# Kernel tuning notes

Measured on AMD Instinct MI355X. Metric: run time of the kernel, lower is better.

Reference implementation:

```python
import jax, jax.numpy as jnp
import numpy as np

EPS = 1e-7

def fake_quant(x, bits):
    """Per-tensor affine fake-quantization (dnn-gating TorchRoundToBits),
    matching torch.fake_quantize_per_tensor_affine with dynamic range."""
    fp_max = jax.lax.stop_gradient(jnp.max(x))
    fp_min = jax.lax.stop_gradient(jnp.min(x))
    qmax = float(2 ** bits - 1)
    qmin = 0.0
    scale = (fp_max - fp_min) / (qmax - qmin) + EPS
    zero_point = jnp.trunc(qmin - fp_min / scale)  # int() cast in torch truncates
    q = jnp.round(x / scale + zero_point)
    qc = jnp.clip(q, qmin, qmax)
    return (qc - zero_point) * scale

def conv2d(x, w, stride=1, padding=1):
    return jax.lax.conv_general_dilated(
        x, w,
        window_strides=(stride, stride),
        padding=[(padding, padding), (padding, padding)],
        dimension_numbers=('NCHW', 'OIHW', 'NCHW'))

def setup_inputs() -> dict:
    key = jax.random.key(0)
    k1, k2 = jax.random.split(key)
    x = jax.random.normal(k1, (32, 256, 56, 56), dtype=jnp.float32)
    # kaiming-like init for a 3x3 conv with 256 in-channels
    fan_in = 256 * 3 * 3
    weight = jax.random.normal(k2, (256, 256, 3, 3), dtype=jnp.float32) / np.sqrt(fan_in)
    return {"x": x, "weight": weight}

def reference(x, weight):
    WBITS, ABITS, PGABITS = 8, 8, 4
    TH = 0.99
    w_q = fake_quant(weight, WBITS)          # quantized weights (shared by both convs)
    msb_in = fake_quant(x, PGABITS)          # low-precision (MSB) input
    msb_out = conv2d(msb_in, w_q)            # [32,256,56,56] prediction pass
    lsb_in = fake_quant(x, ABITS) - msb_in   # residual (LSB) input
    lsb_out = conv2d(lsb_in, w_q)            # high-precision correction pass
    mask = (jax.nn.sigmoid(msb_out) > TH).astype(msb_out.dtype)
    return msb_out + mask * lsb_out
```

## Files before the change

kernel.cpp:

```cpp
#include <hip/hip_runtime.h>
#include <stdint.h>
#include <stddef.h>

typedef int v4i  __attribute__((ext_vector_type(4)));
typedef int v16i __attribute__((ext_vector_type(16)));

struct QParams {
  float s4, z4, s8, z8, sw, zw;
  float s4sw, s8sw;
  int dw;
};

__device__ __forceinline__ unsigned enc_f(float f) {
  unsigned u = __float_as_uint(f);
  return (u & 0x80000000u) ? ~u : (u | 0x80000000u);
}
__device__ __forceinline__ float dec_f(unsigned e) {
  unsigned u = (e & 0x80000000u) ? (e ^ 0x80000000u) : ~e;
  return __uint_as_float(u);
}

__global__ void k_init(unsigned* mm, unsigned* zp) {
  int t = threadIdx.x;
  if (t < 128) zp[t] = 0u;
  if (t == 0) { mm[0] = 0xFFFFFFFFu; mm[1] = 0u; mm[2] = 0xFFFFFFFFu; mm[3] = 0u; }
}

__global__ void k_minmax(const float4* __restrict__ p, int n4, unsigned* mm) {
  float lmin = 3.4e38f, lmax = -3.4e38f;
  for (int i = blockIdx.x * blockDim.x + threadIdx.x; i < n4; i += gridDim.x * blockDim.x) {
    float4 v = p[i];
    lmin = fminf(lmin, fminf(fminf(v.x, v.y), fminf(v.z, v.w)));
    lmax = fmaxf(lmax, fmaxf(fmaxf(v.x, v.y), fmaxf(v.z, v.w)));
  }
  for (int off = 32; off; off >>= 1) {
    lmin = fminf(lmin, __shfl_down(lmin, off, 64));
    lmax = fmaxf(lmax, __shfl_down(lmax, off, 64));
  }
  __shared__ float smin[4], smax[4];
  int w = threadIdx.x >> 6, lane = threadIdx.x & 63;
  if (lane == 0) { smin[w] = lmin; smax[w] = lmax; }
  __syncthreads();
  if (threadIdx.x == 0) {
    float a = fminf(fminf(smin[0], smin[1]), fminf(smin[2], smin[3]));
    float b = fmaxf(fmaxf(smax[0], smax[1]), fmaxf(smax[2], smax[3]));
    atomicMin(&mm[0], enc_f(a));
    atomicMax(&mm[1], enc_f(b));
  }
}

__global__ void k_params(const unsigned* mm, QParams* q) {
  float xmin = dec_f(mm[0]), xmax = dec_f(mm[1]);
  float wmin = dec_f(mm[2]), wmax = dec_f(mm[3]);
  float s4 = (xmax - xmin) / 15.0f + 1e-7f;
  float z4 = truncf(0.0f - xmin / s4);
  float s8 = (xmax - xmin) / 255.0f + 1e-7f;
  float z8 = truncf(0.0f - xmin / s8);
  float sw = (wmax - wmin) / 255.0f + 1e-7f;
  float zw = truncf(0.0f - wmin / sw);
  q->s4 = s4; q->z4 = z4; q->s8 = s8; q->z8 = z8; q->sw = sw; q->zw = zw;
  q->s4sw = s4 * sw; q->s8sw = s8 * sw;
  q->dw = 128 - (int)zw;
}

__global__ void k_quant_w(const float* __restrict__ w, const QParams* __restrict__ q,
                          char* __restrict__ Wc) {
  int t = blockIdx.x * 256 + threadIdx.x;
  float sw = q->sw, zw = q->zw;
  const float* src = w + (size_t)t * 9;
#pragma unroll
  for (int j = 0; j < 9; ++j) {
    float qf = rintf(__fdiv_rn(src[j], sw) + zw);
    qf = fminf(fmaxf(qf, 0.0f), 255.0f);
    Wc[j * 65536 + t] = (char)((int)qf - 128);
  }
}

__global__ void k_quant_x(const float* __restrict__ x, const QParams* __restrict__ q,
                          char* __restrict__ A4, char* __restrict__ A8,
                          int* __restrict__ CS4, int* __restrict__ CS8) {
  __shared__ char sm4[56 * 257];
  __shared__ char sm8[56 * 257];
  __shared__ int cp4[56][4], cp8[56][4];
  int bx = blockIdx.x;
  int n = bx / 56, y = bx % 56;
  int tid = threadIdx.x;
  float s4 = q->s4, z4 = q->z4, s8 = q->s8, z8 = q->z8;
  const float* xrow = x + (size_t)n * 802816 + y * 56;
#pragma unroll 2
  for (int it = 0; it < 56; ++it) {
    int idx = it * 256 + tid;
    int c = idx / 56, xc = idx % 56;
    float v = xrow[(size_t)c * 3136 + xc];
    float q4 = rintf(__fdiv_rn(v, s4) + z4);
    q4 = fminf(fmaxf(q4, 0.0f), 15.0f);
    int t4 = (int)(q4 - z4);
    float q8 = rintf(__fdiv_rn(v, s8) + z8);
    q8 = fminf(fmaxf(q8, 0.0f), 255.0f);
    int t8 = (int)(q8 - z8);
    t8 = max(-128, min(127, t8));
    sm4[xc * 257 + c] = (char)t4;
    sm8[xc * 257 + c] = (char)t8;
  }
  __syncthreads();
  if (tid < 224) {
    int xc = tid >> 2, qq = tid & 3;
    const char* r4 = sm4 + xc * 257 + qq * 64;
    const char* r8 = sm8 + xc * 257 + qq * 64;
    int a = 0, b = 0;
#pragma unroll 8
    for (int c = 0; c < 64; ++c) { a += (signed char)r4[c]; b += (signed char)r8[c]; }
    cp4[xc][qq] = a; cp8[xc][qq] = b;
  }
  __syncthreads();
  int pixbase = n * 3136 + y * 56;
  if (tid < 56) {
    CS4[pixbase + tid] = cp4[tid][0] + cp4[tid][1] + cp4[tid][2] + cp4[tid][3];
    CS8[pixbase + tid] = cp8[tid][0] + cp8[tid][1] + cp8[tid][2] + cp8[tid][3];
  }
  unsigned* A4w = (unsigned*)A4;
  unsigned* A8w = (unsigned*)A8;
#pragma unroll 2
  for (int it = 0; it < 14; ++it) {
    int idx = it * 256 + tid;
    int xc = idx >> 6, wd = idx & 63;
    int sb = xc * 257 + wd * 4;
    unsigned u4 = (unsigned)(unsigned char)sm4[sb]
                | ((unsigned)(unsigned char)sm4[sb + 1] << 8)
                | ((unsigned)(unsigned char)sm4[sb + 2] << 16)
                | ((unsigned)(unsigned char)sm4[sb + 3] << 24);
    unsigned u8 = (unsigned)(unsigned char)sm8[sb]
                | ((unsigned)(unsigned char)sm8[sb + 1] << 8)
                | ((unsigned)(unsigned char)sm8[sb + 2] << 16)
                | ((unsigned)(unsigned char)sm8[sb + 3] << 24);
    size_t o = (size_t)(pixbase + xc) * 64 + wd;
    A4w[o] = u4; A8w[o] = u8;
  }
}

__global__ void k_wsum(const int* __restrict__ CS4, const int* __restrict__ CS8,
                       int* __restrict__ S4, int* __restrict__ S8) {
  int p = blockIdx.x * 256 + threadIdx.x;
  if (p >= 100352) return;
  int rem = p % 3136;
  int y = rem / 56, xc = rem % 56;
  int a = 0, b = 0;
#pragma unroll
  for (int dy = -1; dy <= 1; ++dy) {
    if ((unsigned)(y + dy) >= 56u) continue;
#pragma unroll
    for (int dx = -1; dx <= 1; ++dx) {
      if ((unsigned)(xc + dx) >= 56u) continue;
      int qq = p + dy * 56 + dx;
      a += CS4[qq]; b += CS8[qq];
    }
  }
  S4[p] = a; S8[p] = b;
}

#define GLD16(gp, lp)                                                         \
  __builtin_amdgcn_global_load_lds((const __attribute__((address_space(1))) void*)(gp), \
                                   (__attribute__((address_space(3))) void*)(lp), 16, 0, 0)

__device__ __forceinline__ float pg_merge(int a4v, int a8v, float fs4, float fs8) {
  float msb = fs4 * (float)a4v;
  float c8  = fs8 * (float)a8v;
  float lsb = c8 - msb;
  float sig = 1.0f / (1.0f + expf(-msb));
  return msb + (sig > 0.99f ? lsb : 0.0f);
}

__global__ __launch_bounds__(256, 2) void k_conv(
    const char* __restrict__ A4, const char* __restrict__ A8,
    const char* __restrict__ Wc,
    const int* __restrict__ S4, const int* __restrict__ S8,
    const QParams* __restrict__ q, const char* __restrict__ zpage,
    float* __restrict__ out) {
  __shared__ char smA4[8192], smA8[8192], smB[8192];
  const size_t ASZ = 25690112;
  int tid = threadIdx.x;
  int w = tid >> 6, lane = tid & 63;
  int m0 = blockIdx.x * 128;
  int n0 = blockIdx.y * 128;
  int wm = w >> 1, wn = w & 1;

  int chunk = lane & 3;
  int r0 = (w << 5) + (lane >> 2);
  int r1 = r0 + 16;
  int cg0 = chunk ^ ((r0 >> 1) & 3);
  int cg1 = chunk ^ ((r1 >> 1) & 3);
  int p0 = m0 + r0, p1 = m0 + r1;
  int rem0 = p0 % 3136, rem1 = p1 % 3136;
  int y0 = rem0 / 56, x0 = rem0 % 56;
  int y1 = rem1 / 56, x1 = rem1 % 56;
  const char* aBase0 = A4 + (size_t)p0 * 256 + cg0 * 16;
  const char* aBase1 = A4 + (size_t)p1 * 256 + cg1 * 16;
  const char* bBase0 = Wc + (n0 + r0) * 256 + cg0 * 16;
  const char* bBase1 = Wc + (n0 + r1) * 256 + cg1 * 16;
  const char* zp0 = zpage + chunk * 16;

  char* dA4 = smA4 + (w << 11);
  char* dA8 = smA8 + (w << 11);
  char* dB  = smB  + (w << 11);

  v16i acc4[2][2] = {}, acc8[2][2] = {};
  int r31 = lane & 31, qh = lane >> 5;

  for (int win = 0; win < 9; ++win) {
    int dy = win / 3 - 1, dx = win % 3 - 1;
    int doff = (dy * 56 + dx) * 256;
    bool v0ok = ((unsigned)(y0 + dy) < 56u) && ((unsigned)(x0 + dx) < 56u);
    bool v1ok = ((unsigned)(y1 + dy) < 56u) && ((unsigned)(x1 + dx) < 56u);
    const char* g40 = v0ok ? aBase0 + doff : zp0;
    const char* g41 = v1ok ? aBase1 + doff : zp0;
    const char* g80 = v0ok ? aBase0 + doff + ASZ : zp0;
    const char* g81 = v1ok ? aBase1 + doff + ASZ : zp0;
    const char* gB0 = bBase0 + win * 65536;
    const char* gB1 = bBase1 + win * 65536;
#pragma unroll
    for (int cs = 0; cs < 4; ++cs) {
      int c0 = cs * 64;
      GLD16(g40 + c0, dA4);
      GLD16(g41 + c0, dA4 + 1024);
      GLD16(g80 + c0, dA8);
      GLD16(g81 + c0, dA8 + 1024);
      GLD16(gB0 + c0, dB);
      GLD16(gB1 + c0, dB + 1024);
      asm volatile("s_waitcnt vmcnt(0)" ::: "memory");
      __syncthreads();
#pragma unroll
      for (int kc = 0; kc < 2; ++kc) {
        int ch = kc * 2 + qh;
        v4i a4f[2], a8f[2], bf[2];
#pragma unroll
        for (int fm = 0; fm < 2; ++fm) {
          int row = wm * 64 + fm * 32 + r31;
          int off = row * 64 + ((ch ^ ((row >> 1) & 3)) << 4);
          a4f[fm] = *(const v4i*)(smA4 + off);
          a8f[fm] = *(const v4i*)(smA8 + off);
        }
#pragma unroll
        for (int fn = 0; fn < 2; ++fn) {
          int row = wn * 64 + fn * 32 + r31;
          int off = row * 64 + ((ch ^ ((row >> 1) & 3)) << 4);
          bf[fn] = *(const v4i*)(smB + off);
        }
#pragma unroll
        for (int fm = 0; fm < 2; ++fm)
#pragma unroll
          for (int fn = 0; fn < 2; ++fn) {
            acc4[fm][fn] = __builtin_amdgcn_mfma_i32_32x32x32_i8(a4f[fm], bf[fn], acc4[fm][fn], 0, 0, 0);
            acc8[fm][fn] = __builtin_amdgcn_mfma_i32_32x32x32_i8(a8f[fm], bf[fn], acc8[fm][fn], 0, 0, 0);
          }
      }
      __syncthreads();
    }
  }

  float fs4 = q->s4sw, fs8 = q->s8sw;
  int dwv = q->dw;
#pragma unroll
  for (int fm = 0; fm < 2; ++fm)
#pragma unroll
    for (int fn = 0; fn < 2; ++fn) {
      int kout = n0 + wn * 64 + fn * 32 + r31;
      int pb = m0 + wm * 64 + fm * 32 + 4 * qh;
#pragma unroll
      for (int rg = 0; rg < 4; ++rg) {
        int pr = pb + 8 * rg;
        int4 sv4 = *(const int4*)(S4 + pr);
        int4 sv8 = *(const int4*)(S8 + pr);
        float4 res;
        res.x = pg_merge(acc4[fm][fn][rg * 4 + 0] + dwv * sv4.x,
                         acc8[fm][fn][rg * 4 + 0] + dwv * sv8.x, fs4, fs8);
        res.y = pg_merge(acc4[fm][fn][rg * 4 + 1] + dwv * sv4.y,
                         acc8[fm][fn][rg * 4 + 1] + dwv * sv8.y, fs4, fs8);
        res.z = pg_merge(acc4[fm][fn][rg * 4 + 2] + dwv * sv4.z,
                         acc8[fm][fn][rg * 4 + 2] + dwv * sv8.z, fs4, fs8);
        res.w = pg_merge(acc4[fm][fn][rg * 4 + 3] + dwv * sv4.w,
                         acc8[fm][fn][rg * 4 + 3] + dwv * sv8.w, fs4, fs8);
        int nimg = pr / 3136;
        int rem = pr - nimg * 3136;
        *(float4*)(out + (size_t)nimg * 802816 + (size_t)kout * 3136 + rem) = res;
      }
    }
}

extern "C" void kernel_launch(void* const* d_in, const int* in_sizes, int n_in,
                              void* d_out, int out_size, void* d_ws, size_t ws_size,
                              hipStream_t stream) {
  const float* x  = (const float*)d_in[0];
  const float* wt = (const float*)d_in[1];
  float* out = (float*)d_out;

  char* ws = (char*)d_ws;
  unsigned* mm = (unsigned*)ws;
  QParams* prm = (QParams*)(ws + 64);
  char* zpage = ws + 256;
  char* A4 = ws + 1024;
  const size_t ASZ = 25690112;
  char* A8 = A4 + ASZ;
  int* CS4 = (int*)(A8 + ASZ);
  int* CS8 = CS4 + 100352;
  int* S4  = CS8 + 100352;
  int* S8  = S4 + 100352;
  char* Wc = (char*)(S8 + 100352);

  k_init<<<1, 256, 0, stream>>>(mm, (unsigned*)zpage);
  k_minmax<<<1024, 256, 0, stream>>>((const float4*)x, 25690112 / 4, mm);
  k_minmax<<<64, 256, 0, stream>>>((const float4*)wt, 589824 / 4, mm + 2);
  k_params<<<1, 1, 0, stream>>>(mm, prm);
  k_quant_w<<<256, 256, 0, stream>>>(wt, prm, Wc);
  k_quant_x<<<1792, 256, 0, stream>>>(x, prm, A4, A8, CS4, CS8);
  k_wsum<<<392, 256, 0, stream>>>(CS4, CS8, S4, S8);
  k_conv<<<dim3(784, 2), 256, 0, stream>>>(A4, A8, Wc, S4, S8, prm, zpage, out);
}
```

Measured before the change: 429.2 us.

## Double-buffer conv LDS stages and vectorize quantization kernels

The conv kernel now double-buffers its LDS tiles, issuing the global-to-LDS loads for the next K stage before computing the current one, and waits with partial vmcnt instead of draining. It also precomputes the LDS fragment offsets and packs the window validity into bitmasks. The activation quantizer reads float4 and does word-wide LDS accesses with a 260-byte padded stride, and the weight quantizer now writes coalesced output through shared memory. LDS use for the conv rises to 48KB per block, which may limit occupancy, and the last issued stage loads padding data that is never used.

```diff
diff --git a/kernel.cpp b/kernel.cpp
--- a/kernel.cpp
+++ b/kernel.cpp
@@ -65,51 +65,77 @@
 
 __global__ void k_quant_w(const float* __restrict__ w, const QParams* __restrict__ q,
                           char* __restrict__ Wc) {
-  int t = blockIdx.x * 256 + threadIdx.x;
+  __shared__ char sm[2304];
+  int b = blockIdx.x;
+  int tid = threadIdx.x;
   float sw = q->sw, zw = q->zw;
-  const float* src = w + (size_t)t * 9;
+  const float* src = w + (size_t)b * 2304;
 #pragma unroll
   for (int j = 0; j < 9; ++j) {
-    float qf = rintf(__fdiv_rn(src[j], sw) + zw);
+    int o = j * 256 + tid;
+    float qf = rintf(__fdiv_rn(src[o], sw) + zw);
     qf = fminf(fmaxf(qf, 0.0f), 255.0f);
-    Wc[j * 65536 + t] = (char)((int)qf - 128);
-  }
-}
-
-__global__ void k_quant_x(const float* __restrict__ x, const QParams* __restrict__ q,
+    int c = o / 9, jj = o - c * 9;
+    sm[jj * 256 + c] = (char)((int)qf - 128);
+  }
+  __syncthreads();
+  if (tid < 64) {
+#pragma unroll
+    for (int j = 0; j < 9; ++j)
+      *(unsigned*)(Wc + (size_t)j * 65536 + b * 256 + tid * 4) =
+          *(const unsigned*)(sm + j * 256 + tid * 4);
+  }
+}
+
+__device__ __forceinline__ void quant2(float v, float s4, float z4, float s8, float z8,
+                                       char& o4, char& o8) {
+  float q4 = rintf(__fdiv_rn(v, s4) + z4);
+  q4 = fminf(fmaxf(q4, 0.0f), 15.0f);
+  o4 = (char)(int)(q4 - z4);
+  float q8 = rintf(__fdiv_rn(v, s8) + z8);
+  q8 = fminf(fmaxf(q8, 0.0f), 255.0f);
+  int t8 = (int)(q8 - z8);
+  o8 = (char)max(-128, min(127, t8));
+}
+
+__global__ void k_quant_x(const float4* __restrict__ x4, const QParams* __restrict__ q,
                           char* __restrict__ A4, char* __restrict__ A8,
                           int* __restrict__ CS4, int* __restrict__ CS8) {
-  __shared__ char sm4[56 * 257];
-  __shared__ char sm8[56 * 257];
+  __shared__ char sm4[56 * 260];
+  __shared__ char sm8[56 * 260];
   __shared__ int cp4[56][4], cp8[56][4];
   int bx = blockIdx.x;
   int n = bx / 56, y = bx % 56;
   int tid = threadIdx.x;
   float s4 = q->s4, z4 = q->z4, s8 = q->s8, z8 = q->z8;
-  const float* xrow = x + (size_t)n * 802816 + y * 56;
+  const float4* xrow = x4 + (size_t)n * 200704 + y * 14;
 #pragma unroll 2
-  for (int it = 0; it < 56; ++it) {
+  for (int it = 0; it < 14; ++it) {
     int idx = it * 256 + tid;
-    int c = idx / 56, xc = idx % 56;
-    float v = xrow[(size_t)c * 3136 + xc];
-    float q4 = rintf(__fdiv_rn(v, s4) + z4);
-    q4 = fminf(fmaxf(q4, 0.0f), 15.0f);
-    int t4 = (int)(q4 - z4);
-    float q8 = rintf(__fdiv_rn(v, s8) + z8);
-    q8 = fminf(fmaxf(q8, 0.0f), 255.0f);
-    int t8 = (int)(q8 - z8);
-    t8 = max(-128, min(127, t8));
-    sm4[xc * 257 + c] = (char)t4;
-    sm8[xc * 257 + c] = (char)t8;
+    int c = idx / 14, xq = idx - c * 14;
+    float4 v = xrow[(size_t)c * 784 + xq];
+    int b = (xq * 4) * 260 + c;
+    char a0, b0; quant2(v.x, s4, z4, s8, z8, a0, b0);
+    char a1, b1; quant2(v.y, s4, z4, s8, z8, a1, b1);
+    char a2, b2; quant2(v.z, s4, z4, s8, z8, a2, b2);
+    char a3, b3; quant2(v.w, s4, z4, s8, z8, a3, b3);
+    sm4[b] = a0; sm4[b + 260] = a1; sm4[b + 520] = a2; sm4[b + 780] = a3;
+    sm8[b] = b0; sm8[b + 260] = b1; sm8[b + 520] = b2; sm8[b + 780] = b3;
   }
   __syncthreads();
   if (tid < 224) {
     int xc = tid >> 2, qq = tid & 3;
-    const char* r4 = sm4 + xc * 257 + qq * 64;
-    const char* r8 = sm8 + xc * 257 + qq * 64;
+    const unsigned* r4 = (const unsigned*)(sm4 + xc * 260 + qq * 64);
+    const unsigned* r8 = (const unsigned*)(sm8 + xc * 260 + qq * 64);
     int a = 0, b = 0;
-#pragma unroll 8
-    for (int c = 0; c < 64; ++c) { a += (signed char)r4[c]; b += (signed char)r8[c]; }
+#pragma unroll
+    for (int cw = 0; cw < 16; ++cw) {
+      unsigned u = r4[cw], v = r8[cw];
+      a += (int)(signed char)(u) + (int)(signed char)(u >> 8)
+         + (int)(signed char)(u >> 16) + (int)(signed char)(u >> 24);
+      b += (int)(signed char)(v) + (int)(signed char)(v >> 8)
+         + (int)(signed char)(v >> 16) + (int)(signed char)(v >> 24);
+    }
     cp4[xc][qq] = a; cp8[xc][qq] = b;
   }
   __syncthreads();
@@ -124,17 +150,9 @@
   for (int it = 0; it < 14; ++it) {
     int idx = it * 256 + tid;
     int xc = idx >> 6, wd = idx & 63;
-    int sb = xc * 257 + wd * 4;
-    unsigned u4 = (unsigned)(unsigned char)sm4[sb]
-                | ((unsigned)(unsigned char)sm4[sb + 1] << 8)
-                | ((unsigned)(unsigned char)sm4[sb + 2] << 16)
-                | ((unsigned)(unsigned char)sm4[sb + 3] << 24);
-    unsigned u8 = (unsigned)(unsigned char)sm8[sb]
-                | ((unsigned)(unsigned char)sm8[sb + 1] << 8)
-                | ((unsigned)(unsigned char)sm8[sb + 2] << 16)
-                | ((unsigned)(unsigned char)sm8[sb + 3] << 24);
     size_t o = (size_t)(pixbase + xc) * 64 + wd;
-    A4w[o] = u4; A8w[o] = u8;
+    A4w[o] = *(const unsigned*)(sm4 + xc * 260 + wd * 4);
+    A8w[o] = *(const unsigned*)(sm8 + xc * 260 + wd * 4);
   }
 }
 
@@ -170,13 +188,42 @@
   return msb + (sig > 0.99f ? lsb : 0.0f);
 }
 
+struct StagePtrs {
+  const char* aBase0; const char* aBase1;
+  const char* a8Base0; const char* a8Base1;
+  const char* bBase0; const char* bBase1;
+  const char* zp0;
+  unsigned vm0, vm1;
+};
+
+__device__ __forceinline__ void issue_stage(int s, const StagePtrs& P,
+                                            char* dA4, char* dA8, char* dB) {
+  int win = s >> 2;
+  int cs = (s & 3) << 6;
+  int dy = win / 3 - 1;
+  int dx = win - (dy + 1) * 3 - 1;
+  int doff = (dy * 56 + dx) * 256 + cs;
+  bool ok0 = (P.vm0 >> win) & 1;
+  bool ok1 = (P.vm1 >> win) & 1;
+  const char* g40 = ok0 ? P.aBase0 + doff : P.zp0;
+  const char* g41 = ok1 ? P.aBase1 + doff : P.zp0;
+  const char* g80 = ok0 ? P.a8Base0 + doff : P.zp0;
+  const char* g81 = ok1 ? P.a8Base1 + doff : P.zp0;
+  const char* gB0 = P.bBase0 + win * 65536 + cs;
+  const char* gB1 = P.bBase1 + win * 65536 + cs;
+  if (s >= 36) { gB0 = P.zp0; gB1 = P.zp0; }
+  GLD16(g40, dA4);       GLD16(g41, dA4 + 1024);
+  GLD16(g80, dA8);       GLD16(g81, dA8 + 1024);
+  GLD16(gB0, dB);        GLD16(gB1, dB + 1024);
+}
+
 __global__ __launch_bounds__(256, 2) void k_conv(
     const char* __restrict__ A4, const char* __restrict__ A8,
     const char* __restrict__ Wc,
     const int* __restrict__ S4, const int* __restrict__ S8,
     const QParams* __restrict__ q, const char* __restrict__ zpage,
     float* __restrict__ out) {
-  __shared__ char smA4[8192], smA8[8192], smB[8192];
+  __shared__ char smA4[2][8192], smA8[2][8192], smB[2][8192];
   const size_t ASZ = 25690112;
   int tid = threadIdx.x;
   int w = tid >> 6, lane = tid & 63;
@@ -193,69 +240,90 @@
   int rem0 = p0 % 3136, rem1 = p1 % 3136;
   int y0 = rem0 / 56, x0 = rem0 % 56;
   int y1 = rem1 / 56, x1 = rem1 % 56;
-  const char* aBase0 = A4 + (size_t)p0 * 256 + cg0 * 16;
-  const char* aBase1 = A4 + (size_t)p1 * 256 + cg1 * 16;
-  const char* bBase0 = Wc + (n0 + r0) * 256 + cg0 * 16;
-  const char* bBase1 = Wc + (n0 + r1) * 256 + cg1 * 16;
-  const char* zp0 = zpage + chunk * 16;
-
-  char* dA4 = smA4 + (w << 11);
-  char* dA8 = smA8 + (w << 11);
-  char* dB  = smB  + (w << 11);
+
+  StagePtrs P;
+  P.aBase0 = A4 + (size_t)p0 * 256 + cg0 * 16;
+  P.aBase1 = A4 + (size_t)p1 * 256 + cg1 * 16;
+  P.a8Base0 = P.aBase0 + ASZ;
+  P.a8Base1 = P.aBase1 + ASZ;
+  P.bBase0 = Wc + (n0 + r0) * 256 + cg0 * 16;
+  P.bBase1 = Wc + (n0 + r1) * 256 + cg1 * 16;
+  P.zp0 = zpage + chunk * 16;
+  P.vm0 = 0; P.vm1 = 0;
+#pragma unroll
+  for (int win = 0; win < 9; ++win) {
+    int dy = win / 3 - 1, dx = win % 3 - 1;
+    P.vm0 |= (unsigned)(((unsigned)(y0 + dy) < 56u) & ((unsigned)(x0 + dx) < 56u)) << win;
+    P.vm1 |= (unsigned)(((unsigned)(y1 + dy) < 56u) & ((unsigned)(x1 + dx) < 56u)) << win;
+  }
+
+  char* dA4 = &smA4[0][w << 11];
+  char* dA8 = &smA8[0][w << 11];
+  char* dB  = &smB[0][w << 11];
+  const char* smA4f = &smA4[0][0];
+  const char* smA8f = &smA8[0][0];
+  const char* smBf  = &smB[0][0];
 
   v16i acc4[2][2] = {}, acc8[2][2] = {};
   int r31 = lane & 31, qh = lane >> 5;
 
-  for (int win = 0; win < 9; ++win) {
-    int dy = win / 3 - 1, dx = win % 3 - 1;
-    int doff = (dy * 56 + dx) * 256;
-    bool v0ok = ((unsigned)(y0 + dy) < 56u) && ((unsigned)(x0 + dx) < 56u);
-    bool v1ok = ((unsigned)(y1 + dy) < 56u) && ((unsigned)(x1 + dx) < 56u);
-    const char* g40 = v0ok ? aBase0 + doff : zp0;
-    const char* g41 = v1ok ? aBase1 + doff : zp0;
-    const char* g80 = v0ok ? aBase0 + doff + ASZ : zp0;
-    const char* g81 = v1ok ? aBase1 + doff + ASZ : zp0;
-    const char* gB0 = bBase0 + win * 65536;
-    const char* gB1 = bBase1 + win * 65536;
-#pragma unroll
-    for (int cs = 0; cs < 4; ++cs) {
-      int c0 = cs * 64;
-      GLD16(g40 + c0, dA4);
-      GLD16(g41 + c0, dA4 + 1024);
-      GLD16(g80 + c0, dA8);
-      GLD16(g81 + c0, dA8 + 1024);
-      GLD16(gB0 + c0, dB);
-      GLD16(gB1 + c0, dB + 1024);
-      asm volatile("s_waitcnt vmcnt(0)" ::: "memory");
-      __syncthreads();
-#pragma unroll
-      for (int kc = 0; kc < 2; ++kc) {
-        int ch = kc * 2 + qh;
-        v4i a4f[2], a8f[2], bf[2];
-#pragma unroll
-        for (int fm = 0; fm < 2; ++fm) {
-          int row = wm * 64 + fm * 32 + r31;
-          int off = row * 64 + ((ch ^ ((row >> 1) & 3)) << 4);
-          a4f[fm] = *(const v4i*)(smA4 + off);
-          a8f[fm] = *(const v4i*)(smA8 + off);
-        }
-#pragma unroll
-        for (int fn = 0; fn < 2; ++fn) {
-          int row = wn * 64 + fn * 32 + r31;
-          int off = row * 64 + ((ch ^ ((row >> 1) & 3)) << 4);
-          bf[fn] = *(const v4i*)(smB + off);
-        }
-#pragma unroll
-        for (int fm = 0; fm < 2; ++fm)
-#pragma unroll
-          for (int fn = 0; fn < 2; ++fn) {
-            acc4[fm][fn] = __builtin_amdgcn_mfma_i32_32x32x32_i8(a4f[fm], bf[fn], acc4[fm][fn], 0, 0, 0);
-            acc8[fm][fn] = __builtin_amdgcn_mfma_i32_32x32x32_i8(a8f[fm], bf[fn], acc8[fm][fn], 0, 0, 0);
-          }
-      }
-      __syncthreads();
-    }
-  }
+  int offA[2][2], offB[2][2];
+#pragma unroll
+  for (int fm = 0; fm < 2; ++fm) {
+    int row = wm * 64 + fm * 32 + r31;
+    int swz = (row >> 1) & 3;
+#pragma unroll
+    for (int kc = 0; kc < 2; ++kc)
+      offA[fm][kc] = row * 64 + (((kc * 2 + qh) ^ swz) << 4);
+  }
+#pragma unroll
+  for (int fn = 0; fn < 2; ++fn) {
+    int row = wn * 64 + fn * 32 + r31;
+    int swz = (row >> 1) & 3;
+#pragma unroll
+    for (int kc = 0; kc < 2; ++kc)
+      offB[fn][kc] = row * 64 + (((kc * 2 + qh) ^ swz) << 4);
+  }
+
+#define COMPUTE(BUF)                                                          \
+  {                                                                           \
+    _Pragma("unroll")                                                         \
+    for (int kc = 0; kc < 2; ++kc) {                                          \
+      v4i a4f[2], a8f[2], bf[2];                                              \
+      _Pragma("unroll")                                                       \
+      for (int fm = 0; fm < 2; ++fm) {                                        \
+        a4f[fm] = *(const v4i*)(smA4f + (BUF) * 8192 + offA[fm][kc]);         \
+        a8f[fm] = *(const v4i*)(smA8f + (BUF) * 8192 + offA[fm][kc]);         \
+      }                                                                       \
+      _Pragma("unroll")                                                       \
+      for (int fn = 0; fn < 2; ++fn)                                          \
+        bf[fn] = *(const v4i*)(smBf + (BUF) * 8192 + offB[fn][kc]);           \
+      _Pragma("unroll")                                                       \
+      for (int fm = 0; fm < 2; ++fm)                                          \
+        _Pragma("unroll")                                                     \
+        for (int fn = 0; fn < 2; ++fn) {                                      \
+          acc4[fm][fn] = __builtin_amdgcn_mfma_i32_32x32x32_i8(a4f[fm], bf[fn], acc4[fm][fn], 0, 0, 0); \
+          acc8[fm][fn] = __builtin_amdgcn_mfma_i32_32x32x32_i8(a8f[fm], bf[fn], acc8[fm][fn], 0, 0, 0); \
+        }                                                                     \
+    }                                                                         \
+  }
+
+  issue_stage(0, P, dA4, dA8, dB);
+  for (int sp = 0; sp < 18; ++sp) {
+    int s0 = sp * 2;
+    issue_stage(s0 + 1, P, dA4 + 8192, dA8 + 8192, dB + 8192);
+    asm volatile("s_waitcnt vmcnt(6)" ::: "memory");
+    asm volatile("s_barrier" ::: "memory");
+    COMPUTE(0);
+    asm volatile("s_barrier" ::: "memory");
+    issue_stage(s0 + 2, P, dA4, dA8, dB);
+    asm volatile("s_waitcnt vmcnt(6)" ::: "memory");
+    asm volatile("s_barrier" ::: "memory");
+    COMPUTE(1);
+    asm volatile("s_barrier" ::: "memory");
+  }
+  asm volatile("s_waitcnt vmcnt(0)" ::: "memory");
+#undef COMPUTE
 
   float fs4 = q->s4sw, fs8 = q->s8sw;
   int dwv = q->dw;
@@ -311,7 +379,7 @@
   k_minmax<<<64, 256, 0, stream>>>((const float4*)wt, 589824 / 4, mm + 2);
   k_params<<<1, 1, 0, stream>>>(mm, prm);
   k_quant_w<<<256, 256, 0, stream>>>(wt, prm, Wc);
-  k_quant_x<<<1792, 256, 0, stream>>>(x, prm, A4, A8, CS4, CS8);
+  k_quant_x<<<1792, 256, 0, stream>>>((const float4*)x, prm, A4, A8, CS4, CS8);
   k_wsum<<<392, 256, 0, stream>>>(CS4, CS8, S4, S8);
   k_conv<<<dim3(784, 2), 256, 0, stream>>>(A4, A8, Wc, S4, S8, prm, zpage, out);
 }
```

Result: faster. 420.7 us (-2.0%).
